# Kernel optimization log

Measured on AMD Instinct MI355X. Metric: run time of the kernel, lower is better.

The kernel has to match this reference:

```python
import jax, jax.numpy as jnp
import numpy as np

INPUT = 28
HID = 64
OUT = 10


def setup_inputs() -> dict:
    key = jax.random.key(0)
    ks = jax.random.split(key, 8)
    s_ih = 1.0 / np.sqrt(HID)
    x = jax.random.normal(ks[0], (16384, 28, INPUT), dtype=jnp.float32)
    # PyTorch LSTM params: gate order (i, f, g, o), each block of size HID
    W_ih = jax.random.uniform(ks[1], (4 * HID, INPUT), jnp.float32, -s_ih, s_ih)
    W_hh = jax.random.uniform(ks[2], (4 * HID, HID), jnp.float32, -s_ih, s_ih)
    b_ih = jax.random.uniform(ks[3], (4 * HID,), jnp.float32, -s_ih, s_ih)
    b_hh = jax.random.uniform(ks[4], (4 * HID,), jnp.float32, -s_ih, s_ih)
    s_fc = 1.0 / np.sqrt(HID)
    W_fc = jax.random.uniform(ks[5], (OUT, HID), jnp.float32, -s_fc, s_fc)
    b_fc = jax.random.uniform(ks[6], (OUT,), jnp.float32, -s_fc, s_fc)
    return {"x": x, "W_ih": W_ih, "W_hh": W_hh, "b_ih": b_ih, "b_hh": b_hh,
            "W_fc": W_fc, "b_fc": b_fc}


def reference(x, W_ih, W_hh, b_ih, b_hh, W_fc, b_fc):
    B = x.shape[0]
    # Precompute input projections for all timesteps in one big GEMM: [T, B, 4H]
    x_proj = jnp.einsum('bti,gi->tbg', x, W_ih) + (b_ih + b_hh)

    def step(carry, xp_t):
        h, c = carry
        gates = xp_t + h @ W_hh.T  # [B, 4H]
        i, f, g, o = jnp.split(gates, 4, axis=-1)
        i = jax.nn.sigmoid(i)
        f = jax.nn.sigmoid(f)
        g = jnp.tanh(g)
        o = jax.nn.sigmoid(o)
        c = f * c + i * g
        h = o * jnp.tanh(c)
        return (h, c), None

    h0 = jnp.zeros((B, HID), dtype=x.dtype)
    c0 = jnp.zeros((B, HID), dtype=x.dtype)
    (h_last, _), _ = jax.lax.scan(step, (h0, c0), x_proj)
    # fc on the last timestep's hidden state (== output[:, -1, :])
    return h_last @ W_fc.T + b_fc
```

## Files before the change

kernel.cpp:

```cpp
#include <hip/hip_runtime.h>


namespace {
constexpr int B_TOT   = 16384;
constexpr int T_STEPS = 28;
constexpr int IN_DIM  = 28;
constexpr int HID     = 64;
constexpr int OUT_DIM = 10;
constexpr int ROWS    = 32;
constexpr int THREADS = 512;
constexpr int KPAD    = 104;
constexpr int XROW    = T_STEPS * IN_DIM;
}

typedef __attribute__((ext_vector_type(8))) short short8v;
typedef __attribute__((ext_vector_type(4))) short short4v;
typedef __attribute__((ext_vector_type(4))) float float4v;

__device__ __forceinline__ short f2bf(float f) {
  union { float f; unsigned u; } v; v.f = f;
  unsigned r = v.u + 0x7FFFu + ((v.u >> 16) & 1u);
  return (short)(r >> 16);
}
__device__ __forceinline__ float bf2f(short s) {
  union { unsigned u; float f; } v; v.u = ((unsigned)(unsigned short)s) << 16;
  return v.f;
}
__device__ __forceinline__ float sigf(float v) {
  return __builtin_amdgcn_rcpf(1.0f + __expf(-v));
}
__device__ __forceinline__ float tanh_f(float v) {
  return 2.0f * __builtin_amdgcn_rcpf(1.0f + __expf(-2.0f * v)) - 1.0f;
}

__global__ __launch_bounds__(THREADS, 4)
void lstm_mfma(const float* __restrict__ x, const float* __restrict__ W_ih,
               const float* __restrict__ W_hh, const float* __restrict__ b_ih,
               const float* __restrict__ b_hh, const float* __restrict__ W_fc,
               const float* __restrict__ b_fc, float* __restrict__ out) {
  __shared__ short hs[2][ROWS][KPAD];

  const int tid  = threadIdx.x;
  const int lane = tid & 63;
  const int w    = tid >> 6;
  const int b0   = blockIdx.x * ROWS;
  const int l15  = lane & 15;
  const int q    = lane >> 4;

  short8v a[2][3];
  float4v bias[2];
#pragma unroll
  for (int mtl = 0; mtl < 2; ++mtl) {
    const int mt   = 2 * w + mtl;
    const int m    = 16 * mt + l15;
    const int unit = m >> 2, type = m & 3;
    const int g    = type * 64 + unit;
#pragma unroll
    for (int kc = 0; kc < 3; ++kc) {
      short8v frag;
#pragma unroll
      for (int j = 0; j < 8; ++j) {
        const int k = kc * 32 + q * 8 + j;
        float v = 0.0f;
        if (k < IN_DIM)      v = W_ih[g * IN_DIM + k];
        else if (k >= 32)    v = W_hh[g * HID + (k - 32)];
        frag[j] = f2bf(v);
      }
      a[mtl][kc] = frag;
    }
    const int ub = 4 * mt + q;
    float4v bv;
#pragma unroll
    for (int r = 0; r < 4; ++r) bv[r] = b_ih[r * 64 + ub] + b_hh[r * 64 + ub];
    bias[mtl] = bv;
  }

  const bool xldr = (tid < ROWS * 7);
  const int  xr   = tid / 7;
  const int  xc4  = tid - 7 * xr;

  float4 xv0 = {0.f, 0.f, 0.f, 0.f};
  if (xldr) xv0 = *(const float4*)&x[(b0 + xr) * XROW + 0 * IN_DIM + xc4 * 4];
  for (int idx = tid; idx < 2 * ROWS * KPAD; idx += THREADS)
    (&hs[0][0][0])[idx] = 0;
  __syncthreads();
  if (xldr) {
    short4v s; s[0] = f2bf(xv0.x); s[1] = f2bf(xv0.y); s[2] = f2bf(xv0.z); s[3] = f2bf(xv0.w);
    *(short4v*)&hs[0][xr][xc4 * 4] = s;
  }
  __syncthreads();

  float c_state[2][2] = {{0.f, 0.f}, {0.f, 0.f}};

  for (int t = 0; t < T_STEPS; ++t) {
    const int cur = t & 1, nxt = cur ^ 1;
    const bool hasNext = (t + 1 < T_STEPS);

    float4 xv = {0.f, 0.f, 0.f, 0.f};
    if (hasNext && xldr)
      xv = *(const float4*)&x[(b0 + xr) * XROW + (t + 1) * IN_DIM + xc4 * 4];

    float4v acc[2][2];
#pragma unroll
    for (int mtl = 0; mtl < 2; ++mtl)
#pragma unroll
      for (int nt = 0; nt < 2; ++nt) acc[mtl][nt] = bias[mtl];

#pragma unroll
    for (int kc = 0; kc < 3; ++kc) {
      short8v bf[2];
#pragma unroll
      for (int nt = 0; nt < 2; ++nt)
        bf[nt] = *(const short8v*)&hs[cur][16 * nt + l15][kc * 32 + q * 8];
#pragma unroll
      for (int mtl = 0; mtl < 2; ++mtl)
#pragma unroll
        for (int nt = 0; nt < 2; ++nt)
          acc[mtl][nt] = __builtin_amdgcn_mfma_f32_16x16x32_bf16(
              a[mtl][kc], bf[nt], acc[mtl][nt], 0, 0, 0);
    }

#pragma unroll
    for (int mtl = 0; mtl < 2; ++mtl) {
      const int u = 4 * (2 * w + mtl) + q;
#pragma unroll
      for (int nt = 0; nt < 2; ++nt) {
        float4v g4 = acc[mtl][nt];
        float iv = sigf(g4[0]);
        float fv = sigf(g4[1]);
        float gv = tanh_f(g4[2]);
        float ov = sigf(g4[3]);
        float cn = fv * c_state[mtl][nt] + iv * gv;
        c_state[mtl][nt] = cn;
        float hv = ov * tanh_f(cn);
        hs[nxt][16 * nt + l15][32 + u] = f2bf(hv);
      }
    }

    if (hasNext && xldr) {
      short4v s; s[0] = f2bf(xv.x); s[1] = f2bf(xv.y); s[2] = f2bf(xv.z); s[3] = f2bf(xv.w);
      *(short4v*)&hs[nxt][xr][xc4 * 4] = s;
    }
    __syncthreads();
  }

  if (tid < ROWS * OUT_DIM) {
    const int r = tid / OUT_DIM;
    const int o = tid - r * OUT_DIM;
    float s = b_fc[o];
#pragma unroll
    for (int j = 0; j < HID; ++j)
      s += bf2f(hs[0][r][32 + j]) * W_fc[o * HID + j];
    out[(b0 + r) * OUT_DIM + o] = s;
  }
}

extern "C" void kernel_launch(void* const* d_in, const int* in_sizes, int n_in,
                              void* d_out, int out_size, void* d_ws, size_t ws_size,
                              hipStream_t stream) {
  const float* x    = (const float*)d_in[0];
  const float* W_ih = (const float*)d_in[1];
  const float* W_hh = (const float*)d_in[2];
  const float* b_ih = (const float*)d_in[3];
  const float* b_hh = (const float*)d_in[4];
  const float* W_fc = (const float*)d_in[5];
  const float* b_fc = (const float*)d_in[6];
  float* out = (float*)d_out;

  dim3 grid(B_TOT / ROWS);
  dim3 block(THREADS);
  lstm_mfma<<<grid, block, 0, stream>>>(x, W_ih, W_hh, b_ih, b_hh, W_fc, b_fc, out);
}
```

Baseline: 134.1 us.

## Load x directly into MFMA B-fragments and shrink block to 16 rows

Each block now handles 16 batch rows with 4 waves, and each wave computes 4 M-tiles against a single N-tile. The input timestep is no longer staged through shared memory. Each lane loads its x slice straight into registers, packs it to bf16 with the packed conversion intrinsic, and uses it as the B operand of the first MFMA. Shared memory now holds only the hidden state with a smaller pad. The aim is to cut LDS traffic and per-step work and to raise the block count for better occupancy, at the cost of more MFMA work per wave and more accumulator registers.

New measurement: 160.8 us. +19.9%, slower.

```diff
diff --git a/kernel.cpp b/kernel.cpp
--- a/kernel.cpp
+++ b/kernel.cpp
@@ -1,4 +1,5 @@
 #include <hip/hip_runtime.h>
+#include <hip/hip_bf16.h>
 
 
 namespace {
@@ -7,17 +8,17 @@
 constexpr int IN_DIM  = 28;
 constexpr int HID     = 64;
 constexpr int OUT_DIM = 10;
-constexpr int ROWS    = 32;
-constexpr int THREADS = 512;
-constexpr int KPAD    = 104;
+constexpr int ROWS    = 16;
+constexpr int THREADS = 256;
+constexpr int KP      = 72;
 constexpr int XROW    = T_STEPS * IN_DIM;
 }
 
 typedef __attribute__((ext_vector_type(8))) short short8v;
-typedef __attribute__((ext_vector_type(4))) short short4v;
 typedef __attribute__((ext_vector_type(4))) float float4v;
+typedef __attribute__((ext_vector_type(4))) int   int4v;
 
-__device__ __forceinline__ short f2bf(float f) {
+__device__ __forceinline__ short f2bf_cold(float f) {
   union { float f; unsigned u; } v; v.f = f;
   unsigned r = v.u + 0x7FFFu + ((v.u >> 16) & 1u);
   return (short)(r >> 16);
@@ -25,6 +26,10 @@
 __device__ __forceinline__ float bf2f(short s) {
   union { unsigned u; float f; } v; v.u = ((unsigned)(unsigned short)s) << 16;
   return v.f;
+}
+__device__ __forceinline__ unsigned pk2(float a, float b) {
+  __hip_bfloat162 h = __float22bfloat162_rn(float2{a, b});
+  union { __hip_bfloat162 h; unsigned u; } cv; cv.h = h; return cv.u;
 }
 __device__ __forceinline__ float sigf(float v) {
   return __builtin_amdgcn_rcpf(1.0f + __expf(-v));
@@ -34,24 +39,24 @@
 }
 
 __global__ __launch_bounds__(THREADS, 4)
-void lstm_mfma(const float* __restrict__ x, const float* __restrict__ W_ih,
-               const float* __restrict__ W_hh, const float* __restrict__ b_ih,
-               const float* __restrict__ b_hh, const float* __restrict__ W_fc,
-               const float* __restrict__ b_fc, float* __restrict__ out) {
-  __shared__ short hs[2][ROWS][KPAD];
+void lstm_mfma2(const float* __restrict__ x, const float* __restrict__ W_ih,
+                const float* __restrict__ W_hh, const float* __restrict__ b_ih,
+                const float* __restrict__ b_hh, const float* __restrict__ W_fc,
+                const float* __restrict__ b_fc, float* __restrict__ out) {
+  __shared__ short hs[2][ROWS][KP];
 
   const int tid  = threadIdx.x;
   const int lane = tid & 63;
   const int w    = tid >> 6;
-  const int b0   = blockIdx.x * ROWS;
   const int l15  = lane & 15;
   const int q    = lane >> 4;
+  const int b0   = blockIdx.x * ROWS;
 
-  short8v a[2][3];
-  float4v bias[2];
+  short8v a[4][3];
+  float4v bias[4];
 #pragma unroll
-  for (int mtl = 0; mtl < 2; ++mtl) {
-    const int mt   = 2 * w + mtl;
+  for (int i = 0; i < 4; ++i) {
+    const int mt   = 4 * w + i;
     const int m    = 16 * mt + l15;
     const int unit = m >> 2, type = m & 3;
     const int g    = type * 64 + unit;
@@ -62,85 +67,76 @@
       for (int j = 0; j < 8; ++j) {
         const int k = kc * 32 + q * 8 + j;
         float v = 0.0f;
-        if (k < IN_DIM)      v = W_ih[g * IN_DIM + k];
-        else if (k >= 32)    v = W_hh[g * HID + (k - 32)];
-        frag[j] = f2bf(v);
+        if (k < IN_DIM)   v = W_ih[g * IN_DIM + k];
+        else if (k >= 32) v = W_hh[g * HID + (k - 32)];
+        frag[j] = f2bf_cold(v);
       }
-      a[mtl][kc] = frag;
+      a[i][kc] = frag;
     }
     const int ub = 4 * mt + q;
     float4v bv;
 #pragma unroll
     for (int r = 0; r < 4; ++r) bv[r] = b_ih[r * 64 + ub] + b_hh[r * 64 + ub];
-    bias[mtl] = bv;
+    bias[i] = bv;
   }
 
-  const bool xldr = (tid < ROWS * 7);
-  const int  xr   = tid / 7;
-  const int  xc4  = tid - 7 * xr;
-
-  float4 xv0 = {0.f, 0.f, 0.f, 0.f};
-  if (xldr) xv0 = *(const float4*)&x[(b0 + xr) * XROW + 0 * IN_DIM + xc4 * 4];
-  for (int idx = tid; idx < 2 * ROWS * KPAD; idx += THREADS)
-    (&hs[0][0][0])[idx] = 0;
-  __syncthreads();
-  if (xldr) {
-    short4v s; s[0] = f2bf(xv0.x); s[1] = f2bf(xv0.y); s[2] = f2bf(xv0.z); s[3] = f2bf(xv0.w);
-    *(short4v*)&hs[0][xr][xc4 * 4] = s;
-  }
+  for (int idx = tid; idx < 2 * ROWS * KP; idx += THREADS) (&hs[0][0][0])[idx] = 0;
   __syncthreads();
 
-  float c_state[2][2] = {{0.f, 0.f}, {0.f, 0.f}};
+  const float* xrow = x + (size_t)(b0 + l15) * XROW + q * 8;
+  float4 lo = *(const float4*)xrow;
+  float4 hi = {0.f, 0.f, 0.f, 0.f};
+  if (q < 3) hi = *(const float4*)(xrow + 4);
+
+  float c_state[4] = {0.f, 0.f, 0.f, 0.f};
 
   for (int t = 0; t < T_STEPS; ++t) {
     const int cur = t & 1, nxt = cur ^ 1;
-    const bool hasNext = (t + 1 < T_STEPS);
 
-    float4 xv = {0.f, 0.f, 0.f, 0.f};
-    if (hasNext && xldr)
-      xv = *(const float4*)&x[(b0 + xr) * XROW + (t + 1) * IN_DIM + xc4 * 4];
+    int4v xi;
+    xi[0] = pk2(lo.x, lo.y); xi[1] = pk2(lo.z, lo.w);
+    xi[2] = pk2(hi.x, hi.y); xi[3] = pk2(hi.z, hi.w);
+    union { int4v i; short8v s; } xb; xb.i = xi;
 
-    float4v acc[2][2];
-#pragma unroll
-    for (int mtl = 0; mtl < 2; ++mtl)
-#pragma unroll
-      for (int nt = 0; nt < 2; ++nt) acc[mtl][nt] = bias[mtl];
+    short8v hf0 = *(const short8v*)&hs[cur][l15][q * 8];
+    short8v hf1 = *(const short8v*)&hs[cur][l15][32 + q * 8];
 
-#pragma unroll
-    for (int kc = 0; kc < 3; ++kc) {
-      short8v bf[2];
-#pragma unroll
-      for (int nt = 0; nt < 2; ++nt)
-        bf[nt] = *(const short8v*)&hs[cur][16 * nt + l15][kc * 32 + q * 8];
-#pragma unroll
-      for (int mtl = 0; mtl < 2; ++mtl)
-#pragma unroll
-        for (int nt = 0; nt < 2; ++nt)
-          acc[mtl][nt] = __builtin_amdgcn_mfma_f32_16x16x32_bf16(
-              a[mtl][kc], bf[nt], acc[mtl][nt], 0, 0, 0);
+    if (t + 1 < T_STEPS) {
+      const float* xp = xrow + (t + 1) * IN_DIM;
+      lo = *(const float4*)xp;
+      if (q < 3) hi = *(const float4*)(xp + 4);
     }
 
+    float4v acc[4];
 #pragma unroll
-    for (int mtl = 0; mtl < 2; ++mtl) {
-      const int u = 4 * (2 * w + mtl) + q;
+    for (int i = 0; i < 4; ++i)
+      acc[i] = __builtin_amdgcn_mfma_f32_16x16x32_bf16(a[i][0], xb.s, bias[i], 0, 0, 0);
 #pragma unroll
-      for (int nt = 0; nt < 2; ++nt) {
-        float4v g4 = acc[mtl][nt];
-        float iv = sigf(g4[0]);
-        float fv = sigf(g4[1]);
-        float gv = tanh_f(g4[2]);
-        float ov = sigf(g4[3]);
-        float cn = fv * c_state[mtl][nt] + iv * gv;
-        c_state[mtl][nt] = cn;
-        float hv = ov * tanh_f(cn);
-        hs[nxt][16 * nt + l15][32 + u] = f2bf(hv);
-      }
+    for (int i = 0; i < 4; ++i)
+      acc[i] = __builtin_amdgcn_mfma_f32_16x16x32_bf16(a[i][1], hf0, acc[i], 0, 0, 0);
+#pragma unroll
+    for (int i = 0; i < 4; ++i)
+      acc[i] = __builtin_amdgcn_mfma_f32_16x16x32_bf16(a[i][2], hf1, acc[i], 0, 0, 0);
+
+    float hv[4];
+#pragma unroll
+    for (int i = 0; i < 4; ++i) {
+      float4v g4 = acc[i];
+      float iv = sigf(g4[0]);
+      float fv = sigf(g4[1]);
+      float gv = tanh_f(g4[2]);
+      float ov = sigf(g4[3]);
+      float cn = fv * c_state[i] + iv * gv;
+      c_state[i] = cn;
+      hv[i] = ov * tanh_f(cn);
     }
+    unsigned p01 = pk2(hv[0], hv[1]);
+    unsigned p23 = pk2(hv[2], hv[3]);
+    hs[nxt][l15][16 * w + 0 + q]  = (short)(p01 & 0xFFFF);
+    hs[nxt][l15][16 * w + 4 + q]  = (short)(p01 >> 16);
+    hs[nxt][l15][16 * w + 8 + q]  = (short)(p23 & 0xFFFF);
+    hs[nxt][l15][16 * w + 12 + q] = (short)(p23 >> 16);
 
-    if (hasNext && xldr) {
-      short4v s; s[0] = f2bf(xv.x); s[1] = f2bf(xv.y); s[2] = f2bf(xv.z); s[3] = f2bf(xv.w);
-      *(short4v*)&hs[nxt][xr][xc4 * 4] = s;
-    }
     __syncthreads();
   }
 
@@ -150,7 +146,7 @@
     float s = b_fc[o];
 #pragma unroll
     for (int j = 0; j < HID; ++j)
-      s += bf2f(hs[0][r][32 + j]) * W_fc[o * HID + j];
+      s += bf2f(hs[0][r][j]) * W_fc[o * HID + j];
     out[(b0 + r) * OUT_DIM + o] = s;
   }
 }
@@ -169,5 +165,5 @@
 
   dim3 grid(B_TOT / ROWS);
   dim3 block(THREADS);
-  lstm_mfma<<<grid, block, 0, stream>>>(x, W_ih, W_hh, b_ih, b_hh, W_fc, b_fc, out);
+  lstm_mfma2<<<grid, block, 0, stream>>>(x, W_ih, W_hh, b_ih, b_hh, W_fc, b_fc, out);
 }
```
